# Kernel optimization log

Hardware: AMD Instinct MI355X
Metric: run time of the kernel (lower is better)

The kernel has to match this reference:

```python
import jax, jax.numpy as jnp
from jax import lax
import numpy as np

T = 8
TAU = 2.0       # LIFNode tau
VTH = 1.0       # v_threshold for IF and LIF
ALPHA = 2.0     # surrogate.ATan default alpha
BN_EPS = 1e-5

# --- ATan surrogate-gradient heaviside (spikingjelly semantics) ---
@jax.custom_vjp
def heaviside_atan(x):
    return (x >= 0.0).astype(x.dtype)

def _h_fwd(x):
    return heaviside_atan(x), x

def _h_bwd(x, g):
    sg = (ALPHA / 2.0) / (1.0 + (jnp.pi / 2.0 * ALPHA * x) ** 2)
    return (g * sg,)

heaviside_atan.defvjp(_h_fwd, _h_bwd)

# --- multi-step IF node: v += x; spike; hard reset to 0 ---
def if_node(x_seq):
    def step(v, x):
        v = v + x
        s = heaviside_atan(v - VTH)
        return (1.0 - s) * v, s
    return lax.scan(step, jnp.zeros_like(x_seq[0]), x_seq)[1]

# --- multi-step LIF node (decay_input=True, v_reset=0, hard reset) ---
def lif_node(x_seq):
    def step(v, x):
        v = v + (x - v) / TAU
        s = heaviside_atan(v - VTH)
        return (1.0 - s) * v, s
    return lax.scan(step, jnp.zeros_like(x_seq[0]), x_seq)[1]

def conv2d(x, w, b):
    y = lax.conv_general_dilated(x, w, (1, 1), 'SAME', dimension_numbers=('NCHW', 'OIHW', 'NCHW'))
    return y + b[None, :, None, None]

def bn(x, g, b, m, v):
    scale = g * lax.rsqrt(v + BN_EPS)
    return (x - m[None, :, None, None]) * scale[None, :, None, None] + b[None, :, None, None]

def maxpool2(x):
    return lax.reduce_window(x, -jnp.inf, lax.max, (1, 1, 2, 2), (1, 1, 2, 2), 'VALID')


def setup_inputs():
    key = jax.random.key(0)
    ks = jax.random.split(key, 8)
    B = 32
    f32 = jnp.float32
    d = {}
    d['x'] = jax.random.normal(ks[0], (B, 1, 48, 48), f32)
    d['conv1_w'] = jax.random.normal(ks[1], (128, 1, 3, 3), f32) * 0.2
    d['conv1_b'] = jnp.zeros((128,), f32)
    d['bn1_g'] = jnp.ones((128,), f32)
    d['bn1_b'] = jnp.zeros((128,), f32)
    d['bn1_m'] = jnp.zeros((128,), f32)
    d['bn1_v'] = jnp.ones((128,), f32)
    d['conv2_w'] = jax.random.normal(ks[2], (128, 128, 3, 3), f32) * 0.03
    d['conv2_b'] = jnp.zeros((128,), f32)
    d['bn2_g'] = jnp.ones((128,), f32)
    d['bn2_b'] = jnp.zeros((128,), f32)
    d['bn2_m'] = jnp.zeros((128,), f32)
    d['bn2_v'] = jnp.ones((128,), f32)
    d['fc1_w'] = jax.random.normal(ks[3], (1152, 128 * 12 * 12), f32) * 0.007
    d['fc1_b'] = jnp.zeros((1152,), f32)
    d['fc2_w'] = jax.random.normal(ks[4], (128, 1152), f32) * 0.03
    d['fc2_b'] = jnp.zeros((128,), f32)
    d['fc3_w'] = jax.random.normal(ks[5], (7, 128), f32) * 0.09
    d['fc3_b'] = jnp.zeros((7,), f32)
    return d


def reference(x, conv1_w, conv1_b, bn1_g, bn1_b, bn1_m, bn1_v,
              conv2_w, conv2_b, bn2_g, bn2_b, bn2_m, bn2_v,
              fc1_w, fc1_b, fc2_w, fc2_b, fc3_w, fc3_b):
    B = x.shape[0]
    # layer1 (single-step): conv + BN (eval-mode), dropout is identity at eval
    h = bn(conv2d(x, conv1_w, conv1_b), bn1_g, bn1_b, bn1_m, bn1_v)  # [B,128,48,48]
    # repeat over T timesteps
    x_step = jnp.broadcast_to(h, (T,) + h.shape)                      # [T,B,128,48,48]
    # layer2: IF -> maxpool -> conv -> BN -> IF -> maxpool
    s1 = if_node(x_step)                                              # [T,B,128,48,48]
    p1 = maxpool2(s1.reshape((T * B,) + s1.shape[2:]))                # [T*B,128,24,24]
    c2 = bn(conv2d(p1, conv2_w, conv2_b), bn2_g, bn2_b, bn2_m, bn2_v)
    s2 = if_node(c2.reshape((T, B) + c2.shape[1:]))                   # [T,B,128,24,24]
    p2 = maxpool2(s2.reshape((T * B,) + s2.shape[2:]))                # [T*B,128,12,12]
    # layer3: flatten -> fc -> LIF -> fc -> LIF -> fc -> LIF
    f = p2.reshape(T, B, -1)                                          # [T,B,18432]
    l1 = lif_node(jnp.einsum('tbi,oi->tbo', f, fc1_w) + fc1_b)        # [T,B,1152]
    l2 = lif_node(jnp.einsum('tbi,oi->tbo', l1, fc2_w) + fc2_b)       # [T,B,128]
    l3 = lif_node(jnp.einsum('tbi,oi->tbo', l2, fc3_w) + fc3_b)       # [T,B,7]
    return l3.mean(axis=0)                                            # [B,7]
```

## Files before the change

### kernel.cpp

```cpp
#include <hip/hip_runtime.h>


typedef float  f32x4  __attribute__((ext_vector_type(4)));
typedef __bf16 bf16x8 __attribute__((ext_vector_type(8)));
typedef short  short8 __attribute__((ext_vector_type(8)));

#define T_STEPS 8

static const size_t OFF_P1    = 0;
static const size_t OFF_PART  = 0;
static const size_t OFF_WT    = 44302336;
static const size_t OFF_P2    = 44892160;
static const size_t OFF_W2T   = 54329344;
static const size_t OFF_L1S   = 54919168;
static const size_t OFF_L2PRE = 56098816;

__device__ __forceinline__ unsigned short bf16_rne(float f) {
  unsigned u = __builtin_bit_cast(unsigned, f);
  u += 0x7FFFu + ((u >> 16) & 1u);
  return (unsigned short)(u >> 16);
}
__device__ __forceinline__ float bf16_to_f(unsigned short h) {
  unsigned u = ((unsigned)h) << 16;
  return __builtin_bit_cast(float, u);
}

__device__ __forceinline__ void lds_load16(const void* g, void* l) {
  auto* gp = reinterpret_cast<const __attribute__((address_space(1))) unsigned int*>(
      reinterpret_cast<uintptr_t>(g));
  auto* lp = reinterpret_cast<__attribute__((address_space(3))) unsigned int*>(
      reinterpret_cast<uintptr_t>(l));
  __builtin_amdgcn_global_load_lds(gp, lp, 16, 0, 0);
}

__global__ __launch_bounds__(256) void prep(const float* __restrict__ conv2_w,
                                            const float* __restrict__ fc2_w,
                                            short* __restrict__ wt_hi,
                                            short* __restrict__ wt_lo,
                                            float* __restrict__ w2t,
                                            uint4* __restrict__ p1pad4) {
  int i = blockIdx.x * 256 + threadIdx.x;
  if (i < 147456) {
    int tap = i >> 14;
    int oc  = (i >> 7) & 127;
    int ic  = i & 127;
    float wv = conv2_w[oc * 1152 + ic * 9 + tap];
    unsigned short h = bf16_rne(wv);
    wt_hi[i] = (short)h;
    wt_lo[i] = (short)bf16_rne(wv - bf16_to_f(h));
  } else if (i < 294912) {
    int j = i - 147456;
    int o = j & 127, k = j >> 7;
    w2t[j] = fc2_w[o * 1152 + k];
  } else if (i < 704512) {
    int k = i - 294912;
    int tb = k / 1600;
    int rem = k - tb * 1600;
    int pos = rem >> 4, c8 = rem & 15;
    int y, x;
    if (pos < 26)      { y = 0;  x = pos; }
    else if (pos < 52) { y = 25; x = pos - 26; }
    else { int jj = pos - 52; y = 1 + (jj >> 1); x = (jj & 1) * 25; }
    p1pad4[(tb * 676 + y * 26 + x) * 16 + c8] = make_uint4(0u, 0u, 0u, 0u);
  }
}

__global__ __launch_bounds__(128) void conv1_if_pool(
    const float* __restrict__ x, const float* __restrict__ w1, const float* __restrict__ b1,
    const float* __restrict__ g1, const float* __restrict__ be1, const float* __restrict__ m1,
    const float* __restrict__ vv1, short* __restrict__ p1) {
  __shared__ float patch[16];
  const int c  = threadIdx.x;
  const int sp = blockIdx.x;
  const int b  = blockIdx.y;
  const int oy = sp / 24, ox = sp % 24;
  if (c < 16) {
    int py = c >> 2, px = c & 3;
    int iy = 2 * oy - 1 + py, ix = 2 * ox - 1 + px;
    float v = 0.f;
    if (iy >= 0 && iy < 48 && ix >= 0 && ix < 48) v = x[b * 2304 + iy * 48 + ix];
    patch[c] = v;
  }
  __syncthreads();
  float w[9];
#pragma unroll
  for (int i = 0; i < 9; ++i) w[i] = w1[c * 9 + i];
  float scale = g1[c] * rsqrtf(vv1[c] + 1e-5f);
  float shift = (b1[c] - m1[c]) * scale + be1[c];
  float h[4];
#pragma unroll
  for (int p = 0; p < 4; ++p) {
    int py = p >> 1, px = p & 1;
    float s = 0.f;
#pragma unroll
    for (int dy = 0; dy < 3; ++dy)
#pragma unroll
      for (int dx = 0; dx < 3; ++dx) s += patch[(py + dy) * 4 + (px + dx)] * w[dy * 3 + dx];
    h[p] = s * scale + shift;
  }
  float va = 0.f, vb = 0.f, vc = 0.f, vd = 0.f;
  size_t base = ((size_t)b * 676 + (size_t)(1 + oy) * 26 + (1 + ox)) * 128 + c;
#pragma unroll
  for (int t = 0; t < T_STEPS; ++t) {
    va += h[0]; vb += h[1]; vc += h[2]; vd += h[3];
    bool s0 = va >= 1.f, s1 = vb >= 1.f, s2 = vc >= 1.f, s3 = vd >= 1.f;
    p1[base + (size_t)t * (32 * 676 * 128)] = (s0 | s1 | s2 | s3) ? (short)0x3F80 : (short)0;
    if (s0) va = 0.f; if (s1) vb = 0.f; if (s2) vc = 0.f; if (s3) vd = 0.f;
  }
}

__global__ __launch_bounds__(256) void conv2_gemm(
    const short* __restrict__ p1pad, const short* __restrict__ wt_hi, const short* __restrict__ wt_lo,
    const float* __restrict__ conv2_b, const float* __restrict__ bn2_g, const float* __restrict__ bn2_b,
    const float* __restrict__ bn2_m, const float* __restrict__ bn2_v, short* __restrict__ p2) {
  __shared__ __align__(16) short lds[24576];
  short* ldsA = lds;
  short* ldsBh = lds + 8192;
  short* ldsBl = lds + 16384;

  const int tid = threadIdx.x;
  const int lane = tid & 63;
  const int w = tid >> 6;
  const int wm = w & 1, wn = w >> 1;
  const int b = blockIdx.y;
  const int py = blockIdx.x / 3;
  const int pxq = blockIdx.x - py * 3;

  const int g = (lane & 7) ^ (lane >> 3);
  int rowofs[4], bofs[4];
#pragma unroll
  for (int j = 0; j < 4; ++j) {
    int r = w * 32 + j * 8 + (lane >> 3);
    int t = r >> 4, iy = (r >> 3) & 1, ix = r & 7;
    rowofs[j] = (((t * 32 + b) * 676) + (2 * py + iy) * 26 + (pxq * 8 + ix)) * 128 + g * 8;
    bofs[j] = r * 128 + g * 8;
  }

  f32x4 acc[4][4];
#pragma unroll
  for (int mi = 0; mi < 4; ++mi)
#pragma unroll
    for (int ni = 0; ni < 4; ++ni) acc[mi][ni] = (f32x4){0.f, 0.f, 0.f, 0.f};

#pragma unroll 1
  for (int s = 0; s < 18; ++s) {
    const int tap = s >> 1;
    const int kk = (s & 1) << 6;
    const int tapoff = ((tap / 3) * 26 + (tap % 3)) * 128;
    __syncthreads();
#pragma unroll
    for (int j = 0; j < 4; ++j) {
      lds_load16(p1pad + rowofs[j] + tapoff + kk, ldsA + (w * 32 + j * 8) * 64 + lane * 8);
    }
    const int wtoff = tap * 16384 + kk;
#pragma unroll
    for (int j = 0; j < 4; ++j) {
      lds_load16(wt_hi + wtoff + bofs[j], ldsBh + (w * 32 + j * 8) * 64 + lane * 8);
      lds_load16(wt_lo + wtoff + bofs[j], ldsBl + (w * 32 + j * 8) * 64 + lane * 8);
    }
    __syncthreads();
#pragma unroll
    for (int ks = 0; ks < 2; ++ks) {
      bf16x8 a[4], bh[4], bl[4];
      const int cch = ks * 4 + (lane >> 4);
#pragma unroll
      for (int i = 0; i < 4; ++i) {
        int r = wm * 64 + i * 16 + (lane & 15);
        a[i] = *(const bf16x8*)(ldsA + r * 64 + ((cch ^ (r & 7)) * 8));
        int n = wn * 64 + i * 16 + (lane & 15);
        bh[i] = *(const bf16x8*)(ldsBh + n * 64 + ((cch ^ (n & 7)) * 8));
        bl[i] = *(const bf16x8*)(ldsBl + n * 64 + ((cch ^ (n & 7)) * 8));
      }
#pragma unroll
      for (int mi = 0; mi < 4; ++mi)
#pragma unroll
        for (int ni = 0; ni < 4; ++ni) {
          acc[mi][ni] = __builtin_amdgcn_mfma_f32_16x16x32_bf16(a[mi], bh[ni], acc[mi][ni], 0, 0, 0);
          acc[mi][ni] = __builtin_amdgcn_mfma_f32_16x16x32_bf16(a[mi], bl[ni], acc[mi][ni], 0, 0, 0);
        }
    }
  }

  float sc[4], sh[4];
#pragma unroll
  for (int ni = 0; ni < 4; ++ni) {
    int oc = wn * 64 + ni * 16 + (lane & 15);
    sc[ni] = bn2_g[oc] * rsqrtf(bn2_v[oc] + 1e-5f);
    sh[ni] = (conv2_b[oc] - bn2_m[oc]) * sc[ni] + bn2_b[oc];
  }
  float* ybuf = (float*)lds;
  const int S = 132;
  float vst[16];
#pragma unroll
  for (int q = 0; q < 16; ++q) vst[q] = 0.f;
  unsigned short* p2u = (unsigned short*)p2;
  __syncthreads();
#pragma unroll 1
  for (int half = 0; half < 2; ++half) {
    if (wm == half) {
#pragma unroll
      for (int ni = 0; ni < 4; ++ni)
#pragma unroll
        for (int mi = 0; mi < 4; ++mi)
#pragma unroll
          for (int r = 0; r < 4; ++r) {
            int row = mi * 16 + ((lane >> 4) << 2) + r;
            int col = wn * 64 + ni * 16 + (lane & 15);
            ybuf[row * S + col] = acc[mi][ni][r] * sc[ni] + sh[ni];
          }
    }
    __syncthreads();
    if (tid < 128) {
      const int oc = tid;
#pragma unroll
      for (int tau = 0; tau < 4; ++tau) {
        int t = half * 4 + tau;
        unsigned short ov[4];
#pragma unroll
        for (int gx = 0; gx < 4; ++gx) {
          bool any = false;
#pragma unroll
          for (int iy = 0; iy < 2; ++iy)
#pragma unroll
            for (int j = 0; j < 2; ++j) {
              float xx = ybuf[(tau * 16 + iy * 8 + 2 * gx + j) * S + oc];
              int q = gx * 4 + iy * 2 + j;
              vst[q] += xx;
              bool s = vst[q] >= 1.f;
              any |= s;
              if (s) vst[q] = 0.f;
            }
          ov[gx] = any ? (unsigned short)0x3F80 : (unsigned short)0;
        }
        ushort4 o4; o4.x = ov[0]; o4.y = ov[1]; o4.z = ov[2]; o4.w = ov[3];
        *(ushort4*)(p2u + ((size_t)(t * 32 + b) * 128 + oc) * 144 + py * 12 + pxq * 4) = o4;
      }
    }
    __syncthreads();
  }
}

__global__ __launch_bounds__(512) void fc1_gemm(const short* __restrict__ p2,
                                                const float* __restrict__ fc1_w,
                                                float* __restrict__ part) {
  __shared__ __align__(16) short lds[32768];
  short* ldsA = lds;
  short* ldsBh = lds + 16384;
  short* ldsBl = lds + 24576;

  const int tid = threadIdx.x;
  const int lane = tid & 63;
  const int w = tid >> 6;
  const int wm = w & 3, wn = w >> 2;
  const int n0 = blockIdx.x * 128;
  const int kb = blockIdx.y * 576;

  const int g = (lane & 7) ^ (lane >> 3);
  int aofs[4];
#pragma unroll
  for (int j = 0; j < 4; ++j) {
    int r = w * 32 + j * 8 + (lane >> 3);
    aofs[j] = r * 18432 + g * 8;
  }
  const int bn = tid >> 2;
  const int c0 = (tid & 3) * 2;
  const float* wrow = fc1_w + (size_t)(n0 + bn) * 18432 + c0 * 8;
  const int bpos0 = (c0 ^ (bn & 7)) * 8;
  const int bpos1 = ((c0 + 1) ^ (bn & 7)) * 8;

  f32x4 acc[4][4];
#pragma unroll
  for (int mi = 0; mi < 4; ++mi)
#pragma unroll
    for (int ni = 0; ni < 4; ++ni) acc[mi][ni] = (f32x4){0.f, 0.f, 0.f, 0.f};

#pragma unroll 1
  for (int s = 0; s < 9; ++s) {
    const int koff = kb + s * 64;
    __syncthreads();
#pragma unroll
    for (int j = 0; j < 4; ++j) {
      lds_load16(p2 + aofs[j] + koff, ldsA + (w * 32 + j * 8) * 64 + lane * 8);
    }
    {
      const float4* wp = (const float4*)(wrow + koff);
      float4 q0 = wp[0], q1 = wp[1], q2 = wp[2], q3 = wp[3];
      float fv[16] = {q0.x, q0.y, q0.z, q0.w, q1.x, q1.y, q1.z, q1.w,
                      q2.x, q2.y, q2.z, q2.w, q3.x, q3.y, q3.z, q3.w};
      short8 h0, h1, l0, l1;
#pragma unroll
      for (int q = 0; q < 8; ++q) {
        unsigned short hh = bf16_rne(fv[q]);
        h0[q] = (short)hh;
        l0[q] = (short)bf16_rne(fv[q] - bf16_to_f(hh));
      }
#pragma unroll
      for (int q = 0; q < 8; ++q) {
        unsigned short hh = bf16_rne(fv[8 + q]);
        h1[q] = (short)hh;
        l1[q] = (short)bf16_rne(fv[8 + q] - bf16_to_f(hh));
      }
      *(short8*)(ldsBh + bn * 64 + bpos0) = h0;
      *(short8*)(ldsBh + bn * 64 + bpos1) = h1;
      *(short8*)(ldsBl + bn * 64 + bpos0) = l0;
      *(short8*)(ldsBl + bn * 64 + bpos1) = l1;
    }
    __syncthreads();
#pragma unroll
    for (int ks = 0; ks < 2; ++ks) {
      bf16x8 a[4], bh[4], bl[4];
      const int cch = ks * 4 + (lane >> 4);
#pragma unroll
      for (int i = 0; i < 4; ++i) {
        int r = wm * 64 + i * 16 + (lane & 15);
        a[i] = *(const bf16x8*)(ldsA + r * 64 + ((cch ^ (r & 7)) * 8));
        int n = wn * 64 + i * 16 + (lane & 15);
        bh[i] = *(const bf16x8*)(ldsBh + n * 64 + ((cch ^ (n & 7)) * 8));
        bl[i] = *(const bf16x8*)(ldsBl + n * 64 + ((cch ^ (n & 7)) * 8));
      }
#pragma unroll
      for (int mi = 0; mi < 4; ++mi)
#pragma unroll
        for (int ni = 0; ni < 4; ++ni) {
          acc[mi][ni] = __builtin_amdgcn_mfma_f32_16x16x32_bf16(a[mi], bh[ni], acc[mi][ni], 0, 0, 0);
          acc[mi][ni] = __builtin_amdgcn_mfma_f32_16x16x32_bf16(a[mi], bl[ni], acc[mi][ni], 0, 0, 0);
        }
    }
  }
  const size_t pbase = (size_t)(blockIdx.y * 9 + blockIdx.x) * 32768;
#pragma unroll
  for (int ni = 0; ni < 4; ++ni) {
    int j = wn * 64 + ni * 16 + (lane & 15);
#pragma unroll
    for (int mi = 0; mi < 4; ++mi) {
#pragma unroll
      for (int r = 0; r < 4; ++r) {
        int m = wm * 64 + mi * 16 + ((lane >> 4) << 2) + r;
        part[pbase + (size_t)m * 128 + j] = acc[mi][ni][r];
      }
    }
  }
}

__global__ __launch_bounds__(128) void fc1_reduce_lif(const float* __restrict__ part,
                                                      const float* __restrict__ fc1_b,
                                                      float* __restrict__ l1s) {
  int i = blockIdx.x * 128 + threadIdx.x;
  int b = i / 1152, n = i - b * 1152;
  int nt = n >> 7, j = n & 127;
  float bias = fc1_b[n];
  float v = 0.f;
#pragma unroll
  for (int t = 0; t < T_STEPS; ++t) {
    int m = t * 32 + b;
    float s = bias;
#pragma unroll 8
    for (int ks = 0; ks < 32; ++ks) s += part[(((size_t)ks * 9 + nt) * 256 + m) * 128 + j];
    v += (s - v) * 0.5f;
    bool sp = v >= 1.f;
    l1s[(size_t)m * 1152 + n] = sp ? 1.f : 0.f;
    if (sp) v = 0.f;
  }
}

__global__ __launch_bounds__(128) void fc2_kernel(const float* __restrict__ l1s,
                                                  const float* __restrict__ w2t,
                                                  const float* __restrict__ b2,
                                                  float* __restrict__ l2pre) {
  __shared__ float sx[4608];
  const int tid = threadIdx.x;
  const int m0 = blockIdx.x * 4;
  for (int i = tid; i < 4608; i += 128) sx[i] = l1s[(size_t)m0 * 1152 + i];
  __syncthreads();
  float a0 = 0.f, a1 = 0.f, a2 = 0.f, a3 = 0.f;
  for (int k = 0; k < 1152; ++k) {
    float wv = w2t[k * 128 + tid];
    a0 += sx[k] * wv;
    a1 += sx[1152 + k] * wv;
    a2 += sx[2304 + k] * wv;
    a3 += sx[3456 + k] * wv;
  }
  float bb = b2[tid];
  l2pre[(size_t)(m0 + 0) * 128 + tid] = a0 + bb;
  l2pre[(size_t)(m0 + 1) * 128 + tid] = a1 + bb;
  l2pre[(size_t)(m0 + 2) * 128 + tid] = a2 + bb;
  l2pre[(size_t)(m0 + 3) * 128 + tid] = a3 + bb;
}

__global__ __launch_bounds__(64) void fc3_tail(const float* __restrict__ l2pre,
                                               const float* __restrict__ w3,
                                               const float* __restrict__ b3,
                                               float* __restrict__ out) {
  const int o = blockIdx.x, b = blockIdx.y;
  const int lane = threadIdx.x;
  float wa = w3[o * 128 + lane], wb = w3[o * 128 + 64 + lane];
  float bias = b3[o];
  float va = 0.f, vb = 0.f, v = 0.f, accum = 0.f;
#pragma unroll
  for (int t = 0; t < T_STEPS; ++t) {
    const float* row = l2pre + ((size_t)(t * 32 + b)) * 128;
    float xa = row[lane], xb = row[64 + lane];
    va += (xa - va) * 0.5f;
    bool sa = va >= 1.f; if (sa) va = 0.f;
    vb += (xb - vb) * 0.5f;
    bool sb = vb >= 1.f; if (sb) vb = 0.f;
    float p = (sa ? wa : 0.f) + (sb ? wb : 0.f);
#pragma unroll
    for (int msk = 32; msk > 0; msk >>= 1) p += __shfl_xor(p, msk);
    float xx = p + bias;
    v += (xx - v) * 0.5f;
    bool s = v >= 1.f;
    accum += s ? 1.f : 0.f;
    if (s) v = 0.f;
  }
  if (lane == 0) out[b * 7 + o] = accum * 0.125f;
}

extern "C" void kernel_launch(void* const* d_in, const int* in_sizes, int n_in,
                              void* d_out, int out_size, void* d_ws, size_t ws_size,
                              hipStream_t stream) {
  const float* x       = (const float*)d_in[0];
  const float* conv1_w = (const float*)d_in[1];
  const float* conv1_b = (const float*)d_in[2];
  const float* bn1_g   = (const float*)d_in[3];
  const float* bn1_b   = (const float*)d_in[4];
  const float* bn1_m   = (const float*)d_in[5];
  const float* bn1_v   = (const float*)d_in[6];
  const float* conv2_w = (const float*)d_in[7];
  const float* conv2_b = (const float*)d_in[8];
  const float* bn2_g   = (const float*)d_in[9];
  const float* bn2_b   = (const float*)d_in[10];
  const float* bn2_m   = (const float*)d_in[11];
  const float* bn2_v   = (const float*)d_in[12];
  const float* fc1_w   = (const float*)d_in[13];
  const float* fc1_b   = (const float*)d_in[14];
  const float* fc2_w   = (const float*)d_in[15];
  const float* fc2_b   = (const float*)d_in[16];
  const float* fc3_w   = (const float*)d_in[17];
  const float* fc3_b   = (const float*)d_in[18];

  char* ws = (char*)d_ws;
  short* p1pad = (short*)(ws + OFF_P1);
  float* part  = (float*)(ws + OFF_PART);
  short* wt_hi = (short*)(ws + OFF_WT);
  short* wt_lo = wt_hi + 147456;
  short* p2    = (short*)(ws + OFF_P2);
  float* w2t   = (float*)(ws + OFF_W2T);
  float* l1s   = (float*)(ws + OFF_L1S);
  float* l2pre = (float*)(ws + OFF_L2PRE);
  float* out   = (float*)d_out;

  prep<<<2752, 256, 0, stream>>>(conv2_w, fc2_w, wt_hi, wt_lo, w2t, (uint4*)p1pad);
  conv1_if_pool<<<dim3(576, 32), 128, 0, stream>>>(x, conv1_w, conv1_b, bn1_g, bn1_b, bn1_m, bn1_v, p1pad);
  conv2_gemm<<<dim3(36, 32), 256, 0, stream>>>(p1pad, wt_hi, wt_lo, conv2_b, bn2_g, bn2_b, bn2_m, bn2_v, p2);
  fc1_gemm<<<dim3(9, 32), 512, 0, stream>>>(p2, fc1_w, part);
  fc1_reduce_lif<<<288, 128, 0, stream>>>(part, fc1_b, l1s);
  fc2_kernel<<<64, 128, 0, stream>>>(l1s, w2t, fc2_b, l2pre);
  fc3_tail<<<dim3(7, 32), 64, 0, stream>>>(l2pre, fc3_w, fc3_b, out);
}
```

Baseline: 392.9 us.

## Enlarge conv2 M-tile, vectorize fc1 bf16 split, fuse fc2/fc3 into one tail kernel

The conv2 implicit GEMM now covers a 4x8 spatial patch per block (256 rows instead of 128), doubling accumulator count and halving grid size. This reuses each weight tile across more rows and halves the redundant B-operand loads, at the cost of more registers and LDS per block. The fc1 weight hi/lo bf16 splitting now uses packed bf162 conversion intrinsics instead of scalar bit manipulation. The fc2 and fc3 kernels are merged into one per-batch tail kernel that keeps intermediates in shared memory, removing a launch and a global round-trip.

```diff
diff --git a/kernel.cpp b/kernel.cpp
--- a/kernel.cpp
+++ b/kernel.cpp
@@ -1,19 +1,18 @@
 #include <hip/hip_runtime.h>
+#include <hip/hip_bf16.h>
 
 
 typedef float  f32x4  __attribute__((ext_vector_type(4)));
 typedef __bf16 bf16x8 __attribute__((ext_vector_type(8)));
-typedef short  short8 __attribute__((ext_vector_type(8)));
 
 #define T_STEPS 8
 
 static const size_t OFF_P1    = 0;
 static const size_t OFF_PART  = 0;
 static const size_t OFF_WT    = 44302336;
-static const size_t OFF_P2    = 44892160;
-static const size_t OFF_W2T   = 54329344;
-static const size_t OFF_L1S   = 54919168;
-static const size_t OFF_L2PRE = 56098816;
+static const size_t OFF_P2    = 45481984;
+static const size_t OFF_W2T   = 54919168;
+static const size_t OFF_L1S   = 55508992;
 
 __device__ __forceinline__ unsigned short bf16_rne(float f) {
   unsigned u = __builtin_bit_cast(unsigned, f);
@@ -23,6 +22,17 @@
 __device__ __forceinline__ float bf16_to_f(unsigned short h) {
   unsigned u = ((unsigned)h) << 16;
   return __builtin_bit_cast(float, u);
+}
+
+__device__ __forceinline__ void split_pair(float f0, float f1, unsigned& hi, unsigned& lo) {
+  __hip_bfloat162 h2 = __float22bfloat162_rn(make_float2(f0, f1));
+  unsigned uh; __builtin_memcpy(&uh, &h2, 4);
+  float g0 = __builtin_bit_cast(float, uh << 16);
+  float g1 = __builtin_bit_cast(float, uh & 0xFFFF0000u);
+  __hip_bfloat162 l2 = __float22bfloat162_rn(make_float2(f0 - g0, f1 - g1));
+  unsigned ul; __builtin_memcpy(&ul, &l2, 4);
+  hi = uh;
+  lo = ul;
 }
 
 __device__ __forceinline__ void lds_load16(const void* g, void* l) {
@@ -109,36 +119,40 @@
   }
 }
 
-__global__ __launch_bounds__(256) void conv2_gemm(
+__global__ __launch_bounds__(256, 2) void conv2_gemm(
     const short* __restrict__ p1pad, const short* __restrict__ wt_hi, const short* __restrict__ wt_lo,
     const float* __restrict__ conv2_b, const float* __restrict__ bn2_g, const float* __restrict__ bn2_b,
     const float* __restrict__ bn2_m, const float* __restrict__ bn2_v, short* __restrict__ p2) {
-  __shared__ __align__(16) short lds[24576];
-  short* ldsA = lds;
-  short* ldsBh = lds + 8192;
-  short* ldsBl = lds + 16384;
+  __shared__ __align__(16) short lds[32768];
+  short* ldsA  = lds;
+  short* ldsBh = lds + 16384;
+  short* ldsBl = lds + 24576;
 
   const int tid = threadIdx.x;
   const int lane = tid & 63;
   const int w = tid >> 6;
   const int wm = w & 1, wn = w >> 1;
   const int b = blockIdx.y;
-  const int py = blockIdx.x / 3;
-  const int pxq = blockIdx.x - py * 3;
+  const int gy = blockIdx.x / 3;
+  const int gx = blockIdx.x - gy * 3;
 
   const int g = (lane & 7) ^ (lane >> 3);
-  int rowofs[4], bofs[4];
+  int rowofsA[8], bofs[4];
+#pragma unroll
+  for (int j = 0; j < 8; ++j) {
+    int r = w * 64 + j * 8 + (lane >> 3);
+    int t = r >> 5, iy = (r >> 3) & 3, ix = r & 7;
+    rowofsA[j] = (((t * 32 + b) * 676) + (4 * gy + iy) * 26 + (8 * gx + ix)) * 128 + g * 8;
+  }
 #pragma unroll
   for (int j = 0; j < 4; ++j) {
-    int r = w * 32 + j * 8 + (lane >> 3);
-    int t = r >> 4, iy = (r >> 3) & 1, ix = r & 7;
-    rowofs[j] = (((t * 32 + b) * 676) + (2 * py + iy) * 26 + (pxq * 8 + ix)) * 128 + g * 8;
-    bofs[j] = r * 128 + g * 8;
-  }
-
-  f32x4 acc[4][4];
-#pragma unroll
-  for (int mi = 0; mi < 4; ++mi)
+    int n = w * 32 + j * 8 + (lane >> 3);
+    bofs[j] = n * 128 + g * 8;
+  }
+
+  f32x4 acc[8][4];
+#pragma unroll
+  for (int mi = 0; mi < 8; ++mi)
 #pragma unroll
     for (int ni = 0; ni < 4; ++ni) acc[mi][ni] = (f32x4){0.f, 0.f, 0.f, 0.f};
 
@@ -149,8 +163,8 @@
     const int tapoff = ((tap / 3) * 26 + (tap % 3)) * 128;
     __syncthreads();
 #pragma unroll
-    for (int j = 0; j < 4; ++j) {
-      lds_load16(p1pad + rowofs[j] + tapoff + kk, ldsA + (w * 32 + j * 8) * 64 + lane * 8);
+    for (int j = 0; j < 8; ++j) {
+      lds_load16(p1pad + rowofsA[j] + tapoff + kk, ldsA + (w * 64 + j * 8) * 64 + lane * 8);
     }
     const int wtoff = tap * 16384 + kk;
 #pragma unroll
@@ -161,18 +175,21 @@
     __syncthreads();
 #pragma unroll
     for (int ks = 0; ks < 2; ++ks) {
-      bf16x8 a[4], bh[4], bl[4];
       const int cch = ks * 4 + (lane >> 4);
+      bf16x8 a[8], bh[4], bl[4];
+#pragma unroll
+      for (int i = 0; i < 8; ++i) {
+        int r = wm * 128 + i * 16 + (lane & 15);
+        a[i] = *(const bf16x8*)(ldsA + r * 64 + ((cch ^ (r & 7)) * 8));
+      }
 #pragma unroll
       for (int i = 0; i < 4; ++i) {
-        int r = wm * 64 + i * 16 + (lane & 15);
-        a[i] = *(const bf16x8*)(ldsA + r * 64 + ((cch ^ (r & 7)) * 8));
         int n = wn * 64 + i * 16 + (lane & 15);
         bh[i] = *(const bf16x8*)(ldsBh + n * 64 + ((cch ^ (n & 7)) * 8));
         bl[i] = *(const bf16x8*)(ldsBl + n * 64 + ((cch ^ (n & 7)) * 8));
       }
 #pragma unroll
-      for (int mi = 0; mi < 4; ++mi)
+      for (int mi = 0; mi < 8; ++mi)
 #pragma unroll
         for (int ni = 0; ni < 4; ++ni) {
           acc[mi][ni] = __builtin_amdgcn_mfma_f32_16x16x32_bf16(a[mi], bh[ni], acc[mi][ni], 0, 0, 0);
@@ -190,50 +207,55 @@
   }
   float* ybuf = (float*)lds;
   const int S = 132;
-  float vst[16];
-#pragma unroll
-  for (int q = 0; q < 16; ++q) vst[q] = 0.f;
+  float v[32];
+#pragma unroll
+  for (int q = 0; q < 32; ++q) v[q] = 0.f;
   unsigned short* p2u = (unsigned short*)p2;
   __syncthreads();
 #pragma unroll 1
-  for (int half = 0; half < 2; ++half) {
-    if (wm == half) {
-#pragma unroll
-      for (int ni = 0; ni < 4; ++ni)
-#pragma unroll
-        for (int mi = 0; mi < 4; ++mi)
+  for (int q = 0; q < 4; ++q) {
+    if (wm == (q >> 1)) {
+      const int mib = (q & 1) * 4;
+#pragma unroll
+      for (int ml = 0; ml < 4; ++ml)
+#pragma unroll
+        for (int ni = 0; ni < 4; ++ni)
 #pragma unroll
           for (int r = 0; r < 4; ++r) {
-            int row = mi * 16 + ((lane >> 4) << 2) + r;
+            int lam = ml * 16 + ((lane >> 4) << 2) + r;
             int col = wn * 64 + ni * 16 + (lane & 15);
-            ybuf[row * S + col] = acc[mi][ni][r] * sc[ni] + sh[ni];
+            ybuf[lam * S + col] = acc[mib + ml][ni][r] * sc[ni] + sh[ni];
           }
     }
     __syncthreads();
     if (tid < 128) {
       const int oc = tid;
 #pragma unroll
-      for (int tau = 0; tau < 4; ++tau) {
-        int t = half * 4 + tau;
-        unsigned short ov[4];
-#pragma unroll
-        for (int gx = 0; gx < 4; ++gx) {
-          bool any = false;
-#pragma unroll
-          for (int iy = 0; iy < 2; ++iy)
-#pragma unroll
-            for (int j = 0; j < 2; ++j) {
-              float xx = ybuf[(tau * 16 + iy * 8 + 2 * gx + j) * S + oc];
-              int q = gx * 4 + iy * 2 + j;
-              vst[q] += xx;
-              bool s = vst[q] >= 1.f;
-              any |= s;
-              if (s) vst[q] = 0.f;
-            }
-          ov[gx] = any ? (unsigned short)0x3F80 : (unsigned short)0;
+      for (int tt = 0; tt < 2; ++tt) {
+        int t = 2 * q + tt;
+#pragma unroll
+        for (int pooly = 0; pooly < 2; ++pooly) {
+          unsigned short ov[4];
+#pragma unroll
+          for (int poolx = 0; poolx < 4; ++poolx) {
+            bool any = false;
+#pragma unroll
+            for (int ry = 0; ry < 2; ++ry)
+#pragma unroll
+              for (int rx = 0; rx < 2; ++rx) {
+                int iy = 2 * pooly + ry, ix = 2 * poolx + rx;
+                float xx = ybuf[(tt * 32 + iy * 8 + ix) * S + oc];
+                int qi = iy * 8 + ix;
+                v[qi] += xx;
+                bool ss = v[qi] >= 1.f;
+                any |= ss;
+                if (ss) v[qi] = 0.f;
+              }
+            ov[poolx] = any ? (unsigned short)0x3F80 : (unsigned short)0;
+          }
+          ushort4 o4; o4.x = ov[0]; o4.y = ov[1]; o4.z = ov[2]; o4.w = ov[3];
+          *(ushort4*)(p2u + ((size_t)(t * 32 + b) * 128 + oc) * 144 + (2 * gy + pooly) * 12 + 4 * gx) = o4;
         }
-        ushort4 o4; o4.x = ov[0]; o4.y = ov[1]; o4.z = ov[2]; o4.w = ov[3];
-        *(ushort4*)(p2u + ((size_t)(t * 32 + b) * 128 + oc) * 144 + py * 12 + pxq * 4) = o4;
       }
     }
     __syncthreads();
@@ -285,25 +307,24 @@
     {
       const float4* wp = (const float4*)(wrow + koff);
       float4 q0 = wp[0], q1 = wp[1], q2 = wp[2], q3 = wp[3];
-      float fv[16] = {q0.x, q0.y, q0.z, q0.w, q1.x, q1.y, q1.z, q1.w,
-                      q2.x, q2.y, q2.z, q2.w, q3.x, q3.y, q3.z, q3.w};
-      short8 h0, h1, l0, l1;
-#pragma unroll
-      for (int q = 0; q < 8; ++q) {
-        unsigned short hh = bf16_rne(fv[q]);
-        h0[q] = (short)hh;
-        l0[q] = (short)bf16_rne(fv[q] - bf16_to_f(hh));
-      }
-#pragma unroll
-      for (int q = 0; q < 8; ++q) {
-        unsigned short hh = bf16_rne(fv[8 + q]);
-        h1[q] = (short)hh;
-        l1[q] = (short)bf16_rne(fv[8 + q] - bf16_to_f(hh));
-      }
-      *(short8*)(ldsBh + bn * 64 + bpos0) = h0;
-      *(short8*)(ldsBh + bn * 64 + bpos1) = h1;
-      *(short8*)(ldsBl + bn * 64 + bpos0) = l0;
-      *(short8*)(ldsBl + bn * 64 + bpos1) = l1;
+      unsigned h0, h1, h2, h3, h4, h5, h6, h7;
+      unsigned l0, l1, l2, l3, l4, l5, l6, l7;
+      split_pair(q0.x, q0.y, h0, l0);
+      split_pair(q0.z, q0.w, h1, l1);
+      split_pair(q1.x, q1.y, h2, l2);
+      split_pair(q1.z, q1.w, h3, l3);
+      split_pair(q2.x, q2.y, h4, l4);
+      split_pair(q2.z, q2.w, h5, l5);
+      split_pair(q3.x, q3.y, h6, l6);
+      split_pair(q3.z, q3.w, h7, l7);
+      uint4 H0; H0.x = h0; H0.y = h1; H0.z = h2; H0.w = h3;
+      uint4 H1; H1.x = h4; H1.y = h5; H1.z = h6; H1.w = h7;
+      uint4 L0; L0.x = l0; L0.y = l1; L0.z = l2; L0.w = l3;
+      uint4 L1; L1.x = l4; L1.y = l5; L1.z = l6; L1.w = l7;
+      *(uint4*)(ldsBh + bn * 64 + bpos0) = H0;
+      *(uint4*)(ldsBh + bn * 64 + bpos1) = H1;
+      *(uint4*)(ldsBl + bn * 64 + bpos0) = L0;
+      *(uint4*)(ldsBl + bn * 64 + bpos1) = L1;
     }
     __syncthreads();
 #pragma unroll
@@ -363,57 +384,68 @@
   }
 }
 
-__global__ __launch_bounds__(128) void fc2_kernel(const float* __restrict__ l1s,
-                                                  const float* __restrict__ w2t,
-                                                  const float* __restrict__ b2,
-                                                  float* __restrict__ l2pre) {
-  __shared__ float sx[4608];
+__global__ __launch_bounds__(512) void tail(const float* __restrict__ l1s,
+                                            const float* __restrict__ w2t,
+                                            const float* __restrict__ b2,
+                                            const float* __restrict__ w3,
+                                            const float* __restrict__ b3,
+                                            float* __restrict__ out) {
+  __shared__ float sx[8][1152];
+  __shared__ float part2[4][8][128];
+  __shared__ float s2[8][128];
+  __shared__ float y3[7][8];
+  const int b = blockIdx.x;
   const int tid = threadIdx.x;
-  const int m0 = blockIdx.x * 4;
-  for (int i = tid; i < 4608; i += 128) sx[i] = l1s[(size_t)m0 * 1152 + i];
-  __syncthreads();
-  float a0 = 0.f, a1 = 0.f, a2 = 0.f, a3 = 0.f;
-  for (int k = 0; k < 1152; ++k) {
-    float wv = w2t[k * 128 + tid];
-    a0 += sx[k] * wv;
-    a1 += sx[1152 + k] * wv;
-    a2 += sx[2304 + k] * wv;
-    a3 += sx[3456 + k] * wv;
-  }
-  float bb = b2[tid];
-  l2pre[(size_t)(m0 + 0) * 128 + tid] = a0 + bb;
-  l2pre[(size_t)(m0 + 1) * 128 + tid] = a1 + bb;
-  l2pre[(size_t)(m0 + 2) * 128 + tid] = a2 + bb;
-  l2pre[(size_t)(m0 + 3) * 128 + tid] = a3 + bb;
-}
-
-__global__ __launch_bounds__(64) void fc3_tail(const float* __restrict__ l2pre,
-                                               const float* __restrict__ w3,
-                                               const float* __restrict__ b3,
-                                               float* __restrict__ out) {
-  const int o = blockIdx.x, b = blockIdx.y;
-  const int lane = threadIdx.x;
-  float wa = w3[o * 128 + lane], wb = w3[o * 128 + 64 + lane];
-  float bias = b3[o];
-  float va = 0.f, vb = 0.f, v = 0.f, accum = 0.f;
-#pragma unroll
-  for (int t = 0; t < T_STEPS; ++t) {
-    const float* row = l2pre + ((size_t)(t * 32 + b)) * 128;
-    float xa = row[lane], xb = row[64 + lane];
-    va += (xa - va) * 0.5f;
-    bool sa = va >= 1.f; if (sa) va = 0.f;
-    vb += (xb - vb) * 0.5f;
-    bool sb = vb >= 1.f; if (sb) vb = 0.f;
-    float p = (sa ? wa : 0.f) + (sb ? wb : 0.f);
-#pragma unroll
-    for (int msk = 32; msk > 0; msk >>= 1) p += __shfl_xor(p, msk);
-    float xx = p + bias;
-    v += (xx - v) * 0.5f;
-    bool s = v >= 1.f;
-    accum += s ? 1.f : 0.f;
-    if (s) v = 0.f;
-  }
-  if (lane == 0) out[b * 7 + o] = accum * 0.125f;
+  for (int i = tid; i < 9216; i += 512) {
+    int t = i / 1152, k = i - t * 1152;
+    sx[t][k] = l1s[(size_t)(t * 32 + b) * 1152 + k];
+  }
+  __syncthreads();
+  const int o = tid & 127, h = tid >> 7;
+  float p[8];
+#pragma unroll
+  for (int t = 0; t < 8; ++t) p[t] = 0.f;
+#pragma unroll 4
+  for (int kk = 0; kk < 288; ++kk) {
+    int k = h * 288 + kk;
+    float wv = w2t[k * 128 + o];
+#pragma unroll
+    for (int t = 0; t < 8; ++t) p[t] += sx[t][k] * wv;
+  }
+#pragma unroll
+  for (int t = 0; t < 8; ++t) part2[h][t][o] = p[t];
+  __syncthreads();
+  if (tid < 128) {
+    float v = 0.f;
+#pragma unroll
+    for (int t = 0; t < 8; ++t) {
+      float xx = part2[0][t][o] + part2[1][t][o] + part2[2][t][o] + part2[3][t][o] + b2[o];
+      v += (xx - v) * 0.5f;
+      bool s = v >= 1.f;
+      s2[t][o] = s ? 1.f : 0.f;
+      if (s) v = 0.f;
+    }
+  }
+  __syncthreads();
+  if (tid < 56) {
+    int oo = tid >> 3, t = tid & 7;
+    float d = 0.f;
+    for (int k = 0; k < 128; ++k) d += s2[t][k] * w3[oo * 128 + k];
+    y3[oo][t] = d + b3[oo];
+  }
+  __syncthreads();
+  if (tid < 7) {
+    float v = 0.f, a = 0.f;
+#pragma unroll
+    for (int t = 0; t < 8; ++t) {
+      float xx = y3[tid][t];
+      v += (xx - v) * 0.5f;
+      bool s = v >= 1.f;
+      a += s ? 1.f : 0.f;
+      if (s) v = 0.f;
+    }
+    out[b * 7 + tid] = a * 0.125f;
+  }
 }
 
 extern "C" void kernel_launch(void* const* d_in, const int* in_sizes, int n_in,
@@ -447,14 +479,12 @@
   short* p2    = (short*)(ws + OFF_P2);
   float* w2t   = (float*)(ws + OFF_W2T);
   float* l1s   = (float*)(ws + OFF_L1S);
-  float* l2pre = (float*)(ws + OFF_L2PRE);
   float* out   = (float*)d_out;
 
   prep<<<2752, 256, 0, stream>>>(conv2_w, fc2_w, wt_hi, wt_lo, w2t, (uint4*)p1pad);
   conv1_if_pool<<<dim3(576, 32), 128, 0, stream>>>(x, conv1_w, conv1_b, bn1_g, bn1_b, bn1_m, bn1_v, p1pad);
-  conv2_gemm<<<dim3(36, 32), 256, 0, stream>>>(p1pad, wt_hi, wt_lo, conv2_b, bn2_g, bn2_b, bn2_m, bn2_v, p2);
+  conv2_gemm<<<dim3(18, 32), 256, 0, stream>>>(p1pad, wt_hi, wt_lo, conv2_b, bn2_g, bn2_b, bn2_m, bn2_v, p2);
   fc1_gemm<<<dim3(9, 32), 512, 0, stream>>>(p2, fc1_w, part);
   fc1_reduce_lif<<<288, 128, 0, stream>>>(part, fc1_b, l1s);
-  fc2_kernel<<<64, 128, 0, stream>>>(l1s, w2t, fc2_b, l2pre);
-  fc3_tail<<<dim3(7, 32), 64, 0, stream>>>(l2pre, fc3_w, fc3_b, out);
-}
+  tail<<<32, 512, 0, stream>>>(l1s, w2t, fc2_b, fc3_w, fc3_b, out);
+}
```

Result: slower. 606.9 us (+54.5%).
